# Performance work log

Hardware: AMD Instinct MI355X
Metric: run time of the kernel (lower is better)

## Reference

```python
import jax, jax.numpy as jnp
import numpy as np

D_MODEL = 128
D_STATE = 16
D_CONV = 2
EXPAND = 2
D_INNER = EXPAND * D_MODEL  # 256
DT_RANK = (D_MODEL + 15) // 16  # 8
GROUPS = 4
EPS = 1e-5


def setup_inputs() -> dict:
    key = jax.random.key(0)
    ks = jax.random.split(key, 12)
    s = lambda k, shape, sc=0.02: jax.random.normal(k, shape, dtype=jnp.float32) * sc
    inp = {
        "x_hsi": jax.random.normal(ks[0], (8, D_MODEL, 64, 64), dtype=jnp.float32),
        "W_in": s(ks[1], (D_MODEL, 2 * D_INNER)),            # in_proj (no bias)
        "conv_w": s(ks[2], (D_INNER, D_CONV), 0.5),          # depthwise causal conv, k=2
        "conv_b": s(ks[3], (D_INNER,), 0.1),
        "W_x": s(ks[4], (D_INNER, DT_RANK + 2 * D_STATE)),   # x_proj (no bias)
        "W_dt": s(ks[5], (DT_RANK, D_INNER), 0.1),
        "b_dt": s(ks[6], (D_INNER,), 0.1),
        "A_log": jnp.log(jnp.broadcast_to(jnp.arange(1, D_STATE + 1, dtype=jnp.float32), (D_INNER, D_STATE))),
        "D": jnp.ones((D_INNER,), dtype=jnp.float32),
        "W_out": s(ks[7], (D_INNER, D_MODEL)),               # out_proj (no bias)
        "gn_gamma": jnp.ones((D_MODEL,), dtype=jnp.float32),
        "gn_beta": jnp.zeros((D_MODEL,), dtype=jnp.float32),
    }
    return inp


def _causal_conv_k2(x, w, b):
    # x: [B, L, Din]; w: [Din, 2]; causal depthwise conv, kernel size 2
    xp = jnp.pad(x, ((0, 0), (1, 0), (0, 0)))
    return xp[:, :-1] * w[:, 0] + xp[:, 1:] * w[:, 1] + b


def _selective_scan(xc, dt, Bmat, Cmat, A, D):
    # xc,dt: [B,L,Din]; Bmat,Cmat: [B,L,N]; A: [Din,N]; D: [Din]
    def step(h, inp):
        dt_t, B_t, C_t, x_t = inp          # [B,Din],[B,N],[B,N],[B,Din]
        dA = jnp.exp(dt_t[..., None] * A)                      # [B,Din,N]
        dBx = dt_t[..., None] * B_t[:, None, :] * x_t[..., None]
        h = dA * h + dBx
        y = jnp.einsum('bdn,bn->bd', h, C_t)
        return h, y

    B_, L, Din = xc.shape
    h0 = jnp.zeros((B_, Din, A.shape[1]), dtype=xc.dtype)
    xs = (jnp.swapaxes(dt, 0, 1), jnp.swapaxes(Bmat, 0, 1),
          jnp.swapaxes(Cmat, 0, 1), jnp.swapaxes(xc, 0, 1))
    _, ys = jax.lax.scan(step, h0, xs)     # ys: [L,B,Din]
    return jnp.swapaxes(ys, 0, 1) + xc * D


def _mamba(x, W_in, conv_w, conv_b, W_x, W_dt, b_dt, A_log, D, W_out):
    # x: [B, L, d_model]
    xz = x @ W_in                                   # [B,L,2*Din]
    xh, z = jnp.split(xz, 2, axis=-1)
    xh = jax.nn.silu(_causal_conv_k2(xh, conv_w, conv_b))
    x_dbl = xh @ W_x                                # [B,L,dt_rank+2N]
    dt_low = x_dbl[..., :DT_RANK]
    Bmat = x_dbl[..., DT_RANK:DT_RANK + D_STATE]
    Cmat = x_dbl[..., DT_RANK + D_STATE:]
    dt = jax.nn.softplus(dt_low @ W_dt + b_dt)      # [B,L,Din]
    A = -jnp.exp(A_log)
    y = _selective_scan(xh, dt, Bmat, Cmat, A, D)
    y = y * jax.nn.silu(z)
    return y @ W_out


def _group_norm(x, gamma, beta):
    # x: [B,C,H,W]
    B_, C, H, W = x.shape
    xr = x.reshape(B_, GROUPS, -1)
    mean = xr.mean(-1, keepdims=True)
    var = xr.var(-1, keepdims=True)
    xn = ((xr - mean) * jax.lax.rsqrt(var + EPS)).reshape(B_, C, H, W)
    return xn * gamma[:, None, None] + beta[:, None, None]


def reference(x_hsi, W_in, conv_w, conv_b, W_x, W_dt, b_dt, A_log, D, W_out, gn_gamma, gn_beta):
    B_, C, H, W = x_hsi.shape
    x = jnp.transpose(x_hsi, (0, 2, 3, 1)).reshape(B_, H * W, C)
    x = _mamba(x, W_in, conv_w, conv_b, W_x, W_dt, b_dt, A_log, D, W_out)
    x = jnp.transpose(x.reshape(B_, H, W, C), (0, 3, 1, 2))
    x = jax.nn.silu(_group_norm(x, gn_gamma, gn_beta))
    return x + x_hsi
```

## Files before the change

### kernel.cpp

```cpp
#include <hip/hip_runtime.h>
#include <hip/hip_bf16.h>
#include <hip/hip_fp16.h>
#include <math.h>

#define BATCH   8
#define LSEQ    4096
#define CMODEL  128
#define DIN     256
#define NSTATE  16
#define RRANK   8
#define NCH     128
#define TCH     32

typedef __attribute__((ext_vector_type(8))) short short8;
typedef __attribute__((ext_vector_type(4))) float f32x4;
typedef __attribute__((ext_vector_type(2))) float f32x2;

__device__ __forceinline__ float sigmoid_fast(float x) {
    return __builtin_amdgcn_rcpf(1.0f + __expf(-x));
}
__device__ __forceinline__ float silu_fast(float x) { return x * sigmoid_fast(x); }
__device__ __forceinline__ float softplus_fast(float x) {
    return fmaxf(x, 0.0f) + __logf(1.0f + __expf(-fabsf(x)));
}
__device__ __forceinline__ float bf2f(unsigned short u) {
    return __uint_as_float(((unsigned)u) << 16);
}
__device__ __forceinline__ unsigned pk2bf(float a, float b) {
    __hip_bfloat162 t = __float22bfloat162_rn(make_float2(a, b));
    unsigned r;
    __builtin_memcpy(&r, &t, 4);
    return r;
}
__device__ __forceinline__ unsigned short f2bf1(float v) {
    return (unsigned short)pk2bf(v, v);
}

__device__ __forceinline__ void dA_powers2(float dtv, const float* A, bool fast,
                                           f32x2* dA2)
{
    if (fast) {
        float e1 = __expf(dtv * A[0]);
        float e2 = e1 * e1;
        dA2[0] = (f32x2){e1, e2};
        f32x2 e2s = (f32x2){e2, e2};
        #pragma unroll
        for (int j = 1; j < 8; ++j) dA2[j] = dA2[j-1] * e2s;
    } else {
        #pragma unroll
        for (int j = 0; j < 8; ++j)
            dA2[j] = (f32x2){__expf(dtv * A[2*j]), __expf(dtv * A[2*j+1])};
    }
}

#define LSTR 72
#define YSTR 264

__device__ __forceinline__ void tr64_bf(const float* __restrict__ src, int lds,
                                        int r0, int c0,
                                        unsigned short* __restrict__ dst, int ldd)
{
    __shared__ float ts[64][65];
    const int tid = threadIdx.x;
    #pragma unroll
    for (int it = 0; it < 4; ++it) {
        int slot = tid + it * 256;
        int i = slot >> 4, j4 = slot & 15;
        float4 v = *(const float4*)&src[(size_t)(r0 + i) * lds + c0 + j4 * 4];
        ts[i][j4*4+0] = v.x; ts[i][j4*4+1] = v.y;
        ts[i][j4*4+2] = v.z; ts[i][j4*4+3] = v.w;
    }
    __syncthreads();
    #pragma unroll
    for (int it = 0; it < 4; ++it) {
        int slot = tid + it * 256;
        int row = slot >> 4, c4 = slot & 15;
        unsigned p0 = pk2bf(ts[c4*4+0][row], ts[c4*4+1][row]);
        unsigned p1 = pk2bf(ts[c4*4+2][row], ts[c4*4+3][row]);
        unsigned long long u = (unsigned long long)p0 | ((unsigned long long)p1 << 32);
        *(unsigned long long*)&dst[(size_t)(c0 + row) * ldd + r0 + c4 * 4] = u;
    }
}

__global__ __launch_bounds__(256) void k0_setup(
    const float* __restrict__ W_in, const float* __restrict__ W_out,
    const float* __restrict__ W_x,
    unsigned short* __restrict__ wtin, unsigned short* __restrict__ wtout,
    unsigned short* __restrict__ wxt, float* __restrict__ part)
{
    const int bid = blockIdx.x;
    if (bid < 16) {
        int ct = bid >> 3, jt = bid & 7;
        tr64_bf(W_in, 512, ct * 64, jt * 64, wtin, 128);
    } else if (bid < 24) {
        int t3 = bid - 16;
        int kt = t3 >> 1, ct = t3 & 1;
        tr64_bf(W_out, 128, kt * 64, ct * 64, wtout, 256);
    } else if (bid == 24) {
        for (int idx = threadIdx.x; idx < 48 * 256; idx += 256) {
            int j = idx >> 8, k = idx & 255;
            float v = (j < 40) ? W_x[k * 40 + j] : 0.0f;
            wxt[(size_t)j * 256 + k] = f2bf1(v);
        }
    } else {
        if (threadIdx.x < 64) part[threadIdx.x] = 0.0f;
    }
}

__global__ __launch_bounds__(512) void k1_gemm_in(
    const float* __restrict__ x_hsi, const unsigned short* __restrict__ wtin,
    unsigned short* __restrict__ xhbf, unsigned short* __restrict__ zbf)
{
    __shared__ __align__(16) unsigned short Abf[128 * LSTR];
    const int tid = threadIdx.x;
    const int R0  = blockIdx.x * 128;
    const int b   = R0 >> 12;
    const int l0  = R0 & 4095;
    const int jbase = blockIdx.y * 256;

    const int w    = tid >> 6;
    const int lane = tid & 63;
    const int lm   = lane & 15;
    const int q    = lane >> 4;
    const int mbase = (w & 1) * 64;
    const int nbase = (w >> 1) * 64;

    f32x4 acc[4][4];
    #pragma unroll
    for (int i = 0; i < 4; ++i)
        #pragma unroll
        for (int j = 0; j < 4; ++j) acc[i][j] = (f32x4){0.f, 0.f, 0.f, 0.f};

    const int cq = tid & 15;
    const int lq = tid >> 4;

    for (int kc = 0; kc < 128; kc += 64) {
        __syncthreads();
        {
            float v[4][4];
            #pragma unroll
            for (int t = 0; t < 4; ++t) {
                float4 f = *(const float4*)&x_hsi[((b * 128 + kc + cq * 4 + t) << 12) + l0 + lq * 4];
                v[t][0] = f.x; v[t][1] = f.y; v[t][2] = f.z; v[t][3] = f.w;
            }
            #pragma unroll
            for (int i = 0; i < 4; ++i) {
                unsigned p0 = pk2bf(v[0][i], v[1][i]);
                unsigned p1 = pk2bf(v[2][i], v[3][i]);
                unsigned long long u = (unsigned long long)p0 | ((unsigned long long)p1 << 32);
                *(unsigned long long*)&Abf[(lq * 4 + i) * LSTR + cq * 4] = u;
            }
        }
        __syncthreads();
        #pragma unroll
        for (int kt = 0; kt < 2; ++kt) {
            short8 af[4], bfr[4];
            #pragma unroll
            for (int mt = 0; mt < 4; ++mt)
                af[mt] = *(const short8*)&Abf[(mbase + mt * 16 + lm) * LSTR + kt * 32 + q * 8];
            #pragma unroll
            for (int nt = 0; nt < 4; ++nt)
                bfr[nt] = *(const short8*)&wtin[(size_t)(jbase + nbase + nt * 16 + lm) * 128 + kc + kt * 32 + q * 8];
            #pragma unroll
            for (int mt = 0; mt < 4; ++mt)
                #pragma unroll
                for (int nt = 0; nt < 4; ++nt)
                    acc[mt][nt] = __builtin_amdgcn_mfma_f32_16x16x32_bf16(
                        af[mt], bfr[nt], acc[mt][nt], 0, 0, 0);
        }
    }

    const bool is_xh = (jbase == 0);
    #pragma unroll
    for (int mt = 0; mt < 4; ++mt) {
        #pragma unroll
        for (int r = 0; r < 4; ++r) {
            int row = R0 + mbase + mt * 16 + q * 4 + r;
            #pragma unroll
            for (int nt = 0; nt < 4; ++nt) {
                int col = nbase + nt * 16 + lm;
                float val = acc[mt][nt][r];
                if (is_xh) xhbf[row * 256 + col] = f2bf1(val);
                else       zbf[row * 256 + col]  = f2bf1(silu_fast(val));
            }
        }
    }
}

__global__ __launch_bounds__(256) void k46_conv_xdbl(
    const unsigned short* __restrict__ xhbf, const float* __restrict__ conv_w,
    const float* __restrict__ conv_b, const unsigned short* __restrict__ wxt,
    float* __restrict__ xdbl, unsigned short* __restrict__ xcbf)
{
    __shared__ float cw0[256], cw1[256], cbs[256];
    __shared__ __align__(16) unsigned short xcb[TCH][YSTR];
    const int tid = threadIdx.x;
    const int chunk = blockIdx.x;
    const int b = blockIdx.y;
    const int R0 = b * LSEQ + chunk * TCH;

    cw0[tid] = conv_w[2 * tid];
    cw1[tid] = conv_w[2 * tid + 1];
    cbs[tid] = conv_b[tid];
    __syncthreads();

    #pragma unroll
    for (int it = 0; it < 8; ++it) {
        int idx = tid + it * 256;
        int r = idx >> 6, qq = idx & 63;
        int row = R0 + r;
        int dd = qq * 4;
        ushort4 cu = *(const ushort4*)&xhbf[(size_t)row * 256 + dd];
        float cur[4] = {bf2f(cu.x), bf2f(cu.y), bf2f(cu.z), bf2f(cu.w)};
        float pv[4] = {0.f, 0.f, 0.f, 0.f};
        if ((row & 4095) != 0) {
            ushort4 pu = *(const ushort4*)&xhbf[(size_t)(row - 1) * 256 + dd];
            pv[0] = bf2f(pu.x); pv[1] = bf2f(pu.y);
            pv[2] = bf2f(pu.z); pv[3] = bf2f(pu.w);
        }
        float o[4];
        #pragma unroll
        for (int e = 0; e < 4; ++e)
            o[e] = silu_fast(pv[e] * cw0[dd+e] + cur[e] * cw1[dd+e] + cbs[dd+e]);
        unsigned p0 = pk2bf(o[0], o[1]), p1 = pk2bf(o[2], o[3]);
        unsigned long long u = (unsigned long long)p0 | ((unsigned long long)p1 << 32);
        *(unsigned long long*)&xcb[r][dd] = u;
        *(unsigned long long*)&xcbf[(size_t)row * 256 + dd] = u;
    }
    __syncthreads();

    const int w    = tid >> 6;
    const int lane = tid & 63;
    const int lm   = lane & 15;
    const int q    = lane >> 4;
    const int mt  = w & 1;
    const int nlo = (w < 2) ? 0 : 2;
    const int nn  = (w < 2) ? 2 : 1;
    f32x4 macc[2];
    macc[0] = (f32x4){0.f,0.f,0.f,0.f};
    macc[1] = (f32x4){0.f,0.f,0.f,0.f};
    for (int kc = 0; kc < 256; kc += 32) {
        short8 af = *(const short8*)&xcb[mt * 16 + lm][kc + q * 8];
        #pragma unroll
        for (int t = 0; t < 2; ++t) {
            if (t < nn) {
                short8 bfr = *(const short8*)&wxt[(size_t)((nlo + t) * 16 + lm) * 256 + kc + q * 8];
                macc[t] = __builtin_amdgcn_mfma_f32_16x16x32_bf16(
                    af, bfr, macc[t], 0, 0, 0);
            }
        }
    }
    #pragma unroll
    for (int t = 0; t < 2; ++t) {
        if (t < nn) {
            #pragma unroll
            for (int r = 0; r < 4; ++r) {
                int row = mt * 16 + q * 4 + r;
                int col = (nlo + t) * 16 + lm;
                if (col < 40)
                    xdbl[(size_t)(R0 + row) * 40 + col] = macc[t][r];
            }
        }
    }
}

__global__ __launch_bounds__(256) void k6_scan1(
    const unsigned short* __restrict__ xcbf, const float* __restrict__ xdbl,
    const float* __restrict__ W_dt, const float* __restrict__ b_dt,
    const float* __restrict__ A_log,
    float* __restrict__ hend, float* __restrict__ dtsg)
{
    const int d = threadIdx.x;
    const int chunk = blockIdx.x;
    const int b = blockIdx.y;
    const int t0 = b * LSEQ + chunk * TCH;

    float A[16];
    #pragma unroll
    for (int qq = 0; qq < 4; ++qq) {
        float4 al = *(const float4*)&A_log[d * 16 + qq * 4];
        A[qq*4+0] = -__expf(al.x); A[qq*4+1] = -__expf(al.y);
        A[qq*4+2] = -__expf(al.z); A[qq*4+3] = -__expf(al.w);
    }
    bool fast = true;
    #pragma unroll
    for (int n = 1; n < 16; ++n)
        fast = fast && (fabsf(A[n] - (n + 1) * A[0]) <= 1e-4f * fabsf(A[n]) + 1e-7f);
    float wdt[8];
    #pragma unroll
    for (int r = 0; r < 8; ++r) wdt[r] = W_dt[r * 256 + d];
    const float bdt = b_dt[d];

    f32x2 h2[8];
    #pragma unroll
    for (int j = 0; j < 8; ++j) h2[j] = (f32x2){0.f, 0.f};
    float dtsum = 0.f;

    #pragma unroll 2
    for (int tt = 0; tt < TCH; ++tt) {
        const int row = t0 + tt;
        float xcv = bf2f(xcbf[(size_t)row * 256 + d]);

        const float* xr = &xdbl[(size_t)row * 40];
        float dl[8], Bv[16];
        *(float4*)&dl[0] = *(const float4*)&xr[0];
        *(float4*)&dl[4] = *(const float4*)&xr[4];
        *(float4*)&Bv[0]  = *(const float4*)&xr[8];
        *(float4*)&Bv[4]  = *(const float4*)&xr[12];
        *(float4*)&Bv[8]  = *(const float4*)&xr[16];
        *(float4*)&Bv[12] = *(const float4*)&xr[20];

        float dtr = bdt;
        #pragma unroll
        for (int r = 0; r < 8; ++r) dtr = fmaf(dl[r], wdt[r], dtr);
        float dtv = softplus_fast(dtr);
        dtsum += dtv;
        float dtx = dtv * xcv;

        f32x2 dA2[8];
        dA_powers2(dtv, A, fast, dA2);
        f32x2 dtx2 = (f32x2){dtx, dtx};
        #pragma unroll
        for (int j = 0; j < 8; ++j) {
            f32x2 Bt2 = (f32x2){Bv[2*j], Bv[2*j+1]};
            h2[j] = dA2[j] * h2[j] + dtx2 * Bt2;
        }
    }

    const float* hf = (const float*)h2;
    const int base = ((b * NCH + chunk) * 256 + d) * 16;
    #pragma unroll
    for (int qq = 0; qq < 4; ++qq)
        *(float4*)&hend[base + qq * 4] = make_float4(hf[qq*4], hf[qq*4+1], hf[qq*4+2], hf[qq*4+3]);
    dtsg[(b * NCH + chunk) * 256 + d] = dtsum;
}

__global__ __launch_bounds__(256) void k7_combine(
    const float* __restrict__ dtsg, const float* __restrict__ A_log,
    float* __restrict__ hx)
{
    const int idx = blockIdx.x * 256 + threadIdx.x;
    const int b = idx >> 12;
    const int rem = idx & 4095;
    const int d = rem >> 4, n = rem & 15;
    const float An = -__expf(A_log[d * 16 + n]);
    const int base = b * NCH * 4096 + rem;
    const int sbase = b * NCH * 256 + d;
    float h = 0.f;
    float Sb[8], Eb[8];
    #pragma unroll
    for (int j = 0; j < 8; ++j) {
        Sb[j] = dtsg[sbase + j * 256];
        Eb[j] = hx[base + j * 4096];
    }
    for (int g = 0; g < NCH / 8; ++g) {
        const int o  = base + g * 32768;
        const int so = sbase + g * 2048;
        float Sn[8] = {0,0,0,0,0,0,0,0}, En[8] = {0,0,0,0,0,0,0,0};
        if (g < NCH / 8 - 1) {
            #pragma unroll
            for (int j = 0; j < 8; ++j) {
                Sn[j] = dtsg[so + 2048 + j * 256];
                En[j] = hx[o + 32768 + j * 4096];
            }
        }
        #pragma unroll
        for (int j = 0; j < 8; ++j) {
            hx[o + j * 4096] = h;
            float P = __expf(Sb[j] * An);
            h = fmaf(P, h, Eb[j]);
        }
        #pragma unroll
        for (int j = 0; j < 8; ++j) { Sb[j] = Sn[j]; Eb[j] = En[j]; }
    }
}

__global__ __launch_bounds__(256) void k89_scan2_gemm_out(
    const unsigned short* __restrict__ xcbf, const float* __restrict__ xdbl,
    const float* __restrict__ W_dt, const float* __restrict__ b_dt,
    const float* __restrict__ A_log, const float* __restrict__ Dvec,
    const float* __restrict__ hin, const unsigned short* __restrict__ zbf,
    const unsigned short* __restrict__ wtout,
    unsigned short* __restrict__ out_bf, float* __restrict__ part)
{
    __shared__ __align__(16) unsigned short Ybf[TCH][YSTR];
    __shared__ float pred[8];
    const int tid = threadIdx.x;
    const int chunk = blockIdx.x;
    const int b = blockIdx.y;
    const int t0 = b * LSEQ + chunk * TCH;

    if (tid < 8) pred[tid] = 0.0f;

    const int d = tid;
    float A[16];
    #pragma unroll
    for (int qq = 0; qq < 4; ++qq) {
        float4 al = *(const float4*)&A_log[d * 16 + qq * 4];
        A[qq*4+0] = -__expf(al.x); A[qq*4+1] = -__expf(al.y);
        A[qq*4+2] = -__expf(al.z); A[qq*4+3] = -__expf(al.w);
    }
    bool fast = true;
    #pragma unroll
    for (int n = 1; n < 16; ++n)
        fast = fast && (fabsf(A[n] - (n + 1) * A[0]) <= 1e-4f * fabsf(A[n]) + 1e-7f);
    float wdt[8];
    #pragma unroll
    for (int r = 0; r < 8; ++r) wdt[r] = W_dt[r * 256 + d];
    const float bdt = b_dt[d];
    const float Dd = Dvec[d];

    f32x2 h2[8];
    {
        const int hbase = ((b * NCH + chunk) * 256 + d) * 16;
        float hf[16];
        #pragma unroll
        for (int qq = 0; qq < 4; ++qq) {
            float4 hv = *(const float4*)&hin[hbase + qq * 4];
            hf[qq*4+0] = hv.x; hf[qq*4+1] = hv.y; hf[qq*4+2] = hv.z; hf[qq*4+3] = hv.w;
        }
        #pragma unroll
        for (int j = 0; j < 8; ++j) h2[j] = (f32x2){hf[2*j], hf[2*j+1]};
    }

    #pragma unroll 2
    for (int tt = 0; tt < TCH; ++tt) {
        const int row = t0 + tt;
        const size_t gi = (size_t)row * 256 + d;
        float xcv = bf2f(xcbf[gi]);

        const float* xr = &xdbl[(size_t)row * 40];
        float dl[8], Bv[16], Cv[16];
        *(float4*)&dl[0] = *(const float4*)&xr[0];
        *(float4*)&dl[4] = *(const float4*)&xr[4];
        *(float4*)&Bv[0]  = *(const float4*)&xr[8];
        *(float4*)&Bv[4]  = *(const float4*)&xr[12];
        *(float4*)&Bv[8]  = *(const float4*)&xr[16];
        *(float4*)&Bv[12] = *(const float4*)&xr[20];
        *(float4*)&Cv[0]  = *(const float4*)&xr[24];
        *(float4*)&Cv[4]  = *(const float4*)&xr[28];
        *(float4*)&Cv[8]  = *(const float4*)&xr[32];
        *(float4*)&Cv[12] = *(const float4*)&xr[36];

        float dtr = bdt;
        #pragma unroll
        for (int r = 0; r < 8; ++r) dtr = fmaf(dl[r], wdt[r], dtr);
        float dtv = softplus_fast(dtr);
        float dtx = dtv * xcv;

        f32x2 dA2[8];
        dA_powers2(dtv, A, fast, dA2);
        f32x2 dtx2 = (f32x2){dtx, dtx};
        f32x2 yv2 = (f32x2){0.f, 0.f};
        #pragma unroll
        for (int j = 0; j < 8; ++j) {
            f32x2 Bt2 = (f32x2){Bv[2*j], Bv[2*j+1]};
            f32x2 Ct2 = (f32x2){Cv[2*j], Cv[2*j+1]};
            h2[j] = dA2[j] * h2[j] + dtx2 * Bt2;
            yv2 = yv2 + h2[j] * Ct2;
        }
        float yv = yv2.x + yv2.y;
        yv = fmaf(Dd, xcv, yv);
        Ybf[tt][d] = f2bf1(yv * bf2f(zbf[gi]));
    }
    __syncthreads();

    const int w    = tid >> 6;
    const int lane = tid & 63;
    const int lm   = lane & 15;
    const int q    = lane >> 4;
    const int mbase = (w & 1) * 64;
    const int nbase = (w >> 1) * 16;

    f32x4 acc[4];
    #pragma unroll
    for (int i = 0; i < 4; ++i) acc[i] = (f32x4){0.f, 0.f, 0.f, 0.f};

    for (int ks = 0; ks < 256; ks += 32) {
        short8 bfr = *(const short8*)&Ybf[nbase + lm][ks + q * 8];
        #pragma unroll
        for (int mt = 0; mt < 4; ++mt) {
            short8 af = *(const short8*)&wtout[(size_t)(mbase + mt * 16 + lm) * 256 + ks + q * 8];
            acc[mt] = __builtin_amdgcn_mfma_f32_16x16x32_bf16(
                af, bfr, acc[mt], 0, 0, 0);
        }
    }

    const int l0 = chunk * TCH;
    #pragma unroll
    for (int mt = 0; mt < 4; ++mt) {
        #pragma unroll
        for (int r = 0; r < 4; ++r) {
            int c = mbase + mt * 16 + q * 4 + r;
            long obase = (long)(b * 128 + c) * 4096 + l0;
            out_bf[obase + nbase + lm] = f2bf1(acc[mt][r]);
        }
    }

    float s0 = 0.f, q0 = 0.f, s1 = 0.f, q1 = 0.f;
    #pragma unroll
    for (int mt = 0; mt < 4; ++mt)
        #pragma unroll
        for (int r = 0; r < 4; ++r) {
            float v = acc[mt][r];
            if (mt < 2) { s0 += v; q0 += v * v; }
            else        { s1 += v; q1 += v * v; }
        }
    #pragma unroll
    for (int off = 32; off > 0; off >>= 1) {
        s0 += __shfl_down(s0, off, 64);
        q0 += __shfl_down(q0, off, 64);
        s1 += __shfl_down(s1, off, 64);
        q1 += __shfl_down(q1, off, 64);
    }
    if (lane == 0) {
        int g0 = mbase >> 5;
        atomicAdd(&pred[g0 * 2],           s0);
        atomicAdd(&pred[g0 * 2 + 1],       q0);
        atomicAdd(&pred[(g0 + 1) * 2],     s1);
        atomicAdd(&pred[(g0 + 1) * 2 + 1], q1);
    }
    __syncthreads();
    if (tid < 8) atomicAdd(&part[b * 8 + tid], pred[tid]);
}

__global__ __launch_bounds__(256) void k10c_apply(
    const unsigned short* __restrict__ out_bf, const float* __restrict__ part,
    const float* __restrict__ gamma, const float* __restrict__ beta,
    const float* __restrict__ x_hsi, float* __restrict__ out)
{
    __shared__ float sstat[64];
    if (threadIdx.x < 32) {
        float S = part[threadIdx.x * 2];
        float Q = part[threadIdx.x * 2 + 1];
        const float inv_n = 1.0f / 131072.0f;
        float mean = S * inv_n;
        float var  = Q * inv_n - mean * mean;
        sstat[threadIdx.x * 2]     = mean;
        sstat[threadIdx.x * 2 + 1] = rsqrtf(var + 1e-5f);
    }
    __syncthreads();
    const int idx4 = blockIdx.x * 256 + threadIdx.x;
    const int flat = idx4 * 4;
    const int c = (flat >> 12) & 127;
    const int b = flat >> 19;
    const int g = c >> 5;
    const float mean = sstat[(b * 4 + g) * 2];
    const float inv  = sstat[(b * 4 + g) * 2 + 1];
    const float ga = gamma[c], be = beta[c];
    ushort4 u = *(const ushort4*)&out_bf[flat];
    float4 r = *(const float4*)&x_hsi[flat];
    float vv[4] = {bf2f(u.x), bf2f(u.y), bf2f(u.z), bf2f(u.w)};
    float rr[4] = {r.x, r.y, r.z, r.w};
    float o[4];
    #pragma unroll
    for (int qq = 0; qq < 4; ++qq) {
        float xn = (vv[qq] - mean) * inv;
        float gv = xn * ga + be;
        o[qq] = silu_fast(gv) + rr[qq];
    }
    *(float4*)&out[flat] = make_float4(o[0], o[1], o[2], o[3]);
}

extern "C" void kernel_launch(void* const* d_in, const int* in_sizes, int n_in,
                              void* d_out, int out_size, void* d_ws, size_t ws_size,
                              hipStream_t stream)
{
    const float* x_hsi  = (const float*)d_in[0];
    const float* W_in   = (const float*)d_in[1];
    const float* conv_w = (const float*)d_in[2];
    const float* conv_b = (const float*)d_in[3];
    const float* W_x    = (const float*)d_in[4];
    const float* W_dt   = (const float*)d_in[5];
    const float* b_dt   = (const float*)d_in[6];
    const float* A_log  = (const float*)d_in[7];
    const float* Dv     = (const float*)d_in[8];
    const float* W_out  = (const float*)d_in[9];
    const float* gnw    = (const float*)d_in[10];
    const float* gnb    = (const float*)d_in[11];

    float* ws = (float*)d_ws;
    unsigned short* xhbf = (unsigned short*)(ws + 0);
    unsigned short* zbf  = (unsigned short*)(ws + 4194304);
    float* xdbl   = ws + 8388608;
    float* hx     = ws + 8716288;
    float* dtsg   = ws + 12910592;
    unsigned short* xcbf   = (unsigned short*)(ws + 13172736);
    unsigned short* out_bf = (unsigned short*)(ws + 17367040);
    float* part   = ws + 19464192;
    unsigned short* wtin  = (unsigned short*)(ws + 19464256);
    unsigned short* wtout = (unsigned short*)(ws + 19497024);
    unsigned short* wxt   = (unsigned short*)(ws + 19513408);
    float* outp   = (float*)d_out;

    k0_setup<<<26, 256, 0, stream>>>(W_in, W_out, W_x, wtin, wtout, wxt, part);
    k1_gemm_in<<<dim3(256, 2), 512, 0, stream>>>(x_hsi, wtin, xhbf, zbf);
    k46_conv_xdbl<<<dim3(NCH, BATCH), 256, 0, stream>>>(
        xhbf, conv_w, conv_b, wxt, xdbl, xcbf);
    k6_scan1<<<dim3(NCH, BATCH), 256, 0, stream>>>(
        xcbf, xdbl, W_dt, b_dt, A_log, hx, dtsg);
    k7_combine<<<128, 256, 0, stream>>>(dtsg, A_log, hx);
    k89_scan2_gemm_out<<<dim3(NCH, BATCH), 256, 0, stream>>>(
        xcbf, xdbl, W_dt, b_dt, A_log, Dv, hx, zbf, wtout, out_bf, part);
    k10c_apply<<<4096, 256, 0, stream>>>(out_bf, part, gnw, gnb, x_hsi, outp);
}
```

Before: 206.0 us.

## Cache softplus dt in fp16 from scan1 and prefetch per-step loads in scan2

The first scan pass now writes the computed softplus dt value for every (row, channel) to a new fp16 workspace buffer. The second scan reads it back instead of recomputing the 8-term dt projection and softplus. Both scan kernels also register-double-buffer their per-timestep xc, z and dt loads in groups of 8 steps, and scan2 gets a launch-bounds occupancy hint. This trades extra global write and read traffic (about 16 MB) and fp16 rounding of dt for less ALU work and better load latency hiding.

```diff
diff --git a/kernel.cpp b/kernel.cpp
--- a/kernel.cpp
+++ b/kernel.cpp
@@ -268,7 +268,8 @@
     const unsigned short* __restrict__ xcbf, const float* __restrict__ xdbl,
     const float* __restrict__ W_dt, const float* __restrict__ b_dt,
     const float* __restrict__ A_log,
-    float* __restrict__ hend, float* __restrict__ dtsg)
+    float* __restrict__ hend, float* __restrict__ dtsg,
+    __half* __restrict__ dtvh)
 {
     const int d = threadIdx.x;
     const int chunk = blockIdx.x;
@@ -291,39 +292,54 @@
     for (int r = 0; r < 8; ++r) wdt[r] = W_dt[r * 256 + d];
     const float bdt = b_dt[d];
 
+    unsigned short xc[2][8];
+    #pragma unroll
+    for (int i = 0; i < 8; ++i)
+        xc[0][i] = xcbf[(size_t)(t0 + i) * 256 + d];
+
     f32x2 h2[8];
     #pragma unroll
     for (int j = 0; j < 8; ++j) h2[j] = (f32x2){0.f, 0.f};
     float dtsum = 0.f;
 
-    #pragma unroll 2
-    for (int tt = 0; tt < TCH; ++tt) {
-        const int row = t0 + tt;
-        float xcv = bf2f(xcbf[(size_t)row * 256 + d]);
-
-        const float* xr = &xdbl[(size_t)row * 40];
-        float dl[8], Bv[16];
-        *(float4*)&dl[0] = *(const float4*)&xr[0];
-        *(float4*)&dl[4] = *(const float4*)&xr[4];
-        *(float4*)&Bv[0]  = *(const float4*)&xr[8];
-        *(float4*)&Bv[4]  = *(const float4*)&xr[12];
-        *(float4*)&Bv[8]  = *(const float4*)&xr[16];
-        *(float4*)&Bv[12] = *(const float4*)&xr[20];
-
-        float dtr = bdt;
-        #pragma unroll
-        for (int r = 0; r < 8; ++r) dtr = fmaf(dl[r], wdt[r], dtr);
-        float dtv = softplus_fast(dtr);
-        dtsum += dtv;
-        float dtx = dtv * xcv;
-
-        f32x2 dA2[8];
-        dA_powers2(dtv, A, fast, dA2);
-        f32x2 dtx2 = (f32x2){dtx, dtx};
-        #pragma unroll
-        for (int j = 0; j < 8; ++j) {
-            f32x2 Bt2 = (f32x2){Bv[2*j], Bv[2*j+1]};
-            h2[j] = dA2[j] * h2[j] + dtx2 * Bt2;
+    #pragma unroll
+    for (int g = 0; g < 4; ++g) {
+        if (g < 3) {
+            #pragma unroll
+            for (int i = 0; i < 8; ++i)
+                xc[(g + 1) & 1][i] = xcbf[(size_t)(t0 + (g + 1) * 8 + i) * 256 + d];
+        }
+        #pragma unroll
+        for (int i = 0; i < 8; ++i) {
+            const int tt = g * 8 + i;
+            const int row = t0 + tt;
+            float xcv = bf2f(xc[g & 1][i]);
+
+            const float* xr = &xdbl[(size_t)row * 40];
+            float dl[8], Bv[16];
+            *(float4*)&dl[0] = *(const float4*)&xr[0];
+            *(float4*)&dl[4] = *(const float4*)&xr[4];
+            *(float4*)&Bv[0]  = *(const float4*)&xr[8];
+            *(float4*)&Bv[4]  = *(const float4*)&xr[12];
+            *(float4*)&Bv[8]  = *(const float4*)&xr[16];
+            *(float4*)&Bv[12] = *(const float4*)&xr[20];
+
+            float dtr = bdt;
+            #pragma unroll
+            for (int r = 0; r < 8; ++r) dtr = fmaf(dl[r], wdt[r], dtr);
+            float dtv = softplus_fast(dtr);
+            dtsum += dtv;
+            float dtx = dtv * xcv;
+            dtvh[(size_t)row * 256 + d] = __float2half(dtv);
+
+            f32x2 dA2[8];
+            dA_powers2(dtv, A, fast, dA2);
+            f32x2 dtx2 = (f32x2){dtx, dtx};
+            #pragma unroll
+            for (int j = 0; j < 8; ++j) {
+                f32x2 Bt2 = (f32x2){Bv[2*j], Bv[2*j+1]};
+                h2[j] = dA2[j] * h2[j] + dtx2 * Bt2;
+            }
         }
     }
 
@@ -375,11 +391,11 @@
     }
 }
 
-__global__ __launch_bounds__(256) void k89_scan2_gemm_out(
+__global__ __launch_bounds__(256, 4) void k89_scan2_gemm_out(
     const unsigned short* __restrict__ xcbf, const float* __restrict__ xdbl,
-    const float* __restrict__ W_dt, const float* __restrict__ b_dt,
-    const float* __restrict__ A_log, const float* __restrict__ Dvec,
-    const float* __restrict__ hin, const unsigned short* __restrict__ zbf,
+    const __half* __restrict__ dtvh, const float* __restrict__ A_log,
+    const float* __restrict__ Dvec, const float* __restrict__ hin,
+    const unsigned short* __restrict__ zbf,
     const unsigned short* __restrict__ wtout,
     unsigned short* __restrict__ out_bf, float* __restrict__ part)
 {
@@ -404,10 +420,6 @@
     #pragma unroll
     for (int n = 1; n < 16; ++n)
         fast = fast && (fabsf(A[n] - (n + 1) * A[0]) <= 1e-4f * fabsf(A[n]) + 1e-7f);
-    float wdt[8];
-    #pragma unroll
-    for (int r = 0; r < 8; ++r) wdt[r] = W_dt[r * 256 + d];
-    const float bdt = b_dt[d];
     const float Dd = Dvec[d];
 
     f32x2 h2[8];
@@ -423,45 +435,63 @@
         for (int j = 0; j < 8; ++j) h2[j] = (f32x2){hf[2*j], hf[2*j+1]};
     }
 
-    #pragma unroll 2
-    for (int tt = 0; tt < TCH; ++tt) {
-        const int row = t0 + tt;
-        const size_t gi = (size_t)row * 256 + d;
-        float xcv = bf2f(xcbf[gi]);
-
-        const float* xr = &xdbl[(size_t)row * 40];
-        float dl[8], Bv[16], Cv[16];
-        *(float4*)&dl[0] = *(const float4*)&xr[0];
-        *(float4*)&dl[4] = *(const float4*)&xr[4];
-        *(float4*)&Bv[0]  = *(const float4*)&xr[8];
-        *(float4*)&Bv[4]  = *(const float4*)&xr[12];
-        *(float4*)&Bv[8]  = *(const float4*)&xr[16];
-        *(float4*)&Bv[12] = *(const float4*)&xr[20];
-        *(float4*)&Cv[0]  = *(const float4*)&xr[24];
-        *(float4*)&Cv[4]  = *(const float4*)&xr[28];
-        *(float4*)&Cv[8]  = *(const float4*)&xr[32];
-        *(float4*)&Cv[12] = *(const float4*)&xr[36];
-
-        float dtr = bdt;
-        #pragma unroll
-        for (int r = 0; r < 8; ++r) dtr = fmaf(dl[r], wdt[r], dtr);
-        float dtv = softplus_fast(dtr);
-        float dtx = dtv * xcv;
-
-        f32x2 dA2[8];
-        dA_powers2(dtv, A, fast, dA2);
-        f32x2 dtx2 = (f32x2){dtx, dtx};
-        f32x2 yv2 = (f32x2){0.f, 0.f};
-        #pragma unroll
-        for (int j = 0; j < 8; ++j) {
-            f32x2 Bt2 = (f32x2){Bv[2*j], Bv[2*j+1]};
-            f32x2 Ct2 = (f32x2){Cv[2*j], Cv[2*j+1]};
-            h2[j] = dA2[j] * h2[j] + dtx2 * Bt2;
-            yv2 = yv2 + h2[j] * Ct2;
-        }
-        float yv = yv2.x + yv2.y;
-        yv = fmaf(Dd, xcv, yv);
-        Ybf[tt][d] = f2bf1(yv * bf2f(zbf[gi]));
+    const unsigned short* dth = (const unsigned short*)dtvh;
+    unsigned short xc[2][8], zb[2][8], dt[2][8];
+    #pragma unroll
+    for (int i = 0; i < 8; ++i) {
+        size_t gi = (size_t)(t0 + i) * 256 + d;
+        xc[0][i] = xcbf[gi];
+        zb[0][i] = zbf[gi];
+        dt[0][i] = dth[gi];
+    }
+
+    #pragma unroll
+    for (int g = 0; g < 4; ++g) {
+        if (g < 3) {
+            #pragma unroll
+            for (int i = 0; i < 8; ++i) {
+                size_t gi = (size_t)(t0 + (g + 1) * 8 + i) * 256 + d;
+                xc[(g + 1) & 1][i] = xcbf[gi];
+                zb[(g + 1) & 1][i] = zbf[gi];
+                dt[(g + 1) & 1][i] = dth[gi];
+            }
+        }
+        #pragma unroll
+        for (int i = 0; i < 8; ++i) {
+            const int tt = g * 8 + i;
+            const int row = t0 + tt;
+            float xcv = bf2f(xc[g & 1][i]);
+            __half hv;
+            __builtin_memcpy(&hv, &dt[g & 1][i], 2);
+            float dtv = __half2float(hv);
+            float dtx = dtv * xcv;
+
+            const float* xr = &xdbl[(size_t)row * 40];
+            float Bv[16], Cv[16];
+            *(float4*)&Bv[0]  = *(const float4*)&xr[8];
+            *(float4*)&Bv[4]  = *(const float4*)&xr[12];
+            *(float4*)&Bv[8]  = *(const float4*)&xr[16];
+            *(float4*)&Bv[12] = *(const float4*)&xr[20];
+            *(float4*)&Cv[0]  = *(const float4*)&xr[24];
+            *(float4*)&Cv[4]  = *(const float4*)&xr[28];
+            *(float4*)&Cv[8]  = *(const float4*)&xr[32];
+            *(float4*)&Cv[12] = *(const float4*)&xr[36];
+
+            f32x2 dA2[8];
+            dA_powers2(dtv, A, fast, dA2);
+            f32x2 dtx2 = (f32x2){dtx, dtx};
+            f32x2 yv2 = (f32x2){0.f, 0.f};
+            #pragma unroll
+            for (int j = 0; j < 8; ++j) {
+                f32x2 Bt2 = (f32x2){Bv[2*j], Bv[2*j+1]};
+                f32x2 Ct2 = (f32x2){Cv[2*j], Cv[2*j+1]};
+                h2[j] = dA2[j] * h2[j] + dtx2 * Bt2;
+                yv2 = yv2 + h2[j] * Ct2;
+            }
+            float yv = yv2.x + yv2.y;
+            yv = fmaf(Dd, xcv, yv);
+            Ybf[tt][d] = f2bf1(yv * bf2f(zb[g & 1][i]));
+        }
     }
     __syncthreads();
 
@@ -591,6 +621,7 @@
     unsigned short* wtin  = (unsigned short*)(ws + 19464256);
     unsigned short* wtout = (unsigned short*)(ws + 19497024);
     unsigned short* wxt   = (unsigned short*)(ws + 19513408);
+    __half* dtvh  = (__half*)(ws + 19519552);
     float* outp   = (float*)d_out;
 
     k0_setup<<<26, 256, 0, stream>>>(W_in, W_out, W_x, wtin, wtout, wxt, part);
@@ -598,9 +629,9 @@
     k46_conv_xdbl<<<dim3(NCH, BATCH), 256, 0, stream>>>(
         xhbf, conv_w, conv_b, wxt, xdbl, xcbf);
     k6_scan1<<<dim3(NCH, BATCH), 256, 0, stream>>>(
-        xcbf, xdbl, W_dt, b_dt, A_log, hx, dtsg);
+        xcbf, xdbl, W_dt, b_dt, A_log, hx, dtsg, dtvh);
     k7_combine<<<128, 256, 0, stream>>>(dtsg, A_log, hx);
     k89_scan2_gemm_out<<<dim3(NCH, BATCH), 256, 0, stream>>>(
-        xcbf, xdbl, W_dt, b_dt, A_log, Dv, hx, zbf, wtout, out_bf, part);
+        xcbf, xdbl, dtvh, A_log, Dv, hx, zbf, wtout, out_bf, part);
     k10c_apply<<<4096, 256, 0, stream>>>(out_bf, part, gnw, gnb, x_hsi, outp);
 }
```

After: 345.4 us. 1.68x slower.
